# Performance work log

Hardware: AMD Instinct MI355X
Metric: run time of the kernel (lower is better)

The kernel has to match this reference:

```python
import jax, jax.numpy as jnp
import numpy as np

HID = 64
NUM_LAYERS = 2
EPS = 1e-5


def _layernorm(x, g, b):
    mu = jnp.mean(x, axis=-1, keepdims=True)
    var = jnp.mean(jnp.square(x - mu), axis=-1, keepdims=True)
    return (x - mu) * jax.lax.rsqrt(var + EPS) * g + b


def _mlp(x, w1, b1, g, beta, w2, b2):
    # Linear -> LayerNorm -> ReLU -> Linear (torch Linear: x @ W.T + b)
    h = x @ w1.T + b1
    h = jax.nn.relu(_layernorm(h, g, beta))
    return h @ w2.T + b2


def _gru(x, h, wih, whh, bih, bhh):
    # PyTorch GRUCell semantics
    gi = x @ wih.T + bih
    gh = h @ whh.T + bhh
    ir, iz, inn = jnp.split(gi, 3, axis=-1)
    hr, hz, hn = jnp.split(gh, 3, axis=-1)
    r = jax.nn.sigmoid(ir + hr)
    z = jax.nn.sigmoid(iz + hz)
    n = jnp.tanh(inn + r * hn)
    return (1.0 - z) * n + z * h


def setup_inputs() -> dict:
    key = jax.random.key(0)
    ks = iter(jax.random.split(key, 64))
    s = 0.05

    def rn(shape):
        return jax.random.normal(next(ks), shape, dtype=jnp.float32) * s

    B, M, K1 = 32, 256, 128
    inp = {
        'hybrid_input': jax.random.normal(next(ks), (B, M, K1, 4), dtype=jnp.float32),
        'hidden_state': jnp.zeros((B, HID), dtype=jnp.float32),
        # input encoder
        'enc_w1': rn((HID, 4)), 'enc_b1': rn((HID,)),
        'enc_g': jnp.ones((HID,), jnp.float32), 'enc_beta': jnp.zeros((HID,), jnp.float32),
        'enc_w2': rn((HID, HID)), 'enc_b2': rn((HID,)),
        # per-layer, per-side (axis0=layer, axis1=[row,col]) params
        'l_w1': rn((NUM_LAYERS, 2, HID, HID)), 'l_b1': rn((NUM_LAYERS, 2, HID)),
        'l_g': jnp.ones((NUM_LAYERS, 2, HID), jnp.float32), 'l_beta': jnp.zeros((NUM_LAYERS, 2, HID), jnp.float32),
        'l_w2': rn((NUM_LAYERS, 2, HID, HID)), 'l_b2': rn((NUM_LAYERS, 2, HID)),
        'l_gwih': rn((NUM_LAYERS, 2, 3 * HID, HID)), 'l_gwhh': rn((NUM_LAYERS, 2, 3 * HID, HID)),
        'l_gbih': rn((NUM_LAYERS, 2, 3 * HID)), 'l_gbhh': rn((NUM_LAYERS, 2, 3 * HID)),
        # top-level GRU
        'g_wih': rn((3 * HID, HID)), 'g_whh': rn((3 * HID, HID)),
        'g_bih': rn((3 * HID,)), 'g_bhh': rn((3 * HID,)),
        # head: Linear(2H->H) -> ReLU -> Linear(H->1)
        'head_w1': rn((HID, 2 * HID)), 'head_b1': rn((HID,)),
        'head_w2': rn((1, HID)), 'head_b2': rn((1,)),
    }
    return inp


def reference(hybrid_input, hidden_state, enc_w1, enc_b1, enc_g, enc_beta, enc_w2, enc_b2,
              l_w1, l_b1, l_g, l_beta, l_w2, l_b2, l_gwih, l_gwhh, l_gbih, l_gbhh,
              g_wih, g_whh, g_bih, g_bhh, head_w1, head_b1, head_w2, head_b2):
    # input encoder
    x = _mlp(hybrid_input, enc_w1, enc_b1, enc_g, enc_beta, enc_w2, enc_b2)

    for l in range(NUM_LAYERS):
        # row pass: max over axis 2 (K+1)
        row_max = jnp.max(x, axis=2, keepdims=True)
        upd = _mlp(x - row_max, l_w1[l, 0], l_b1[l, 0], l_g[l, 0], l_beta[l, 0], l_w2[l, 0], l_b2[l, 0])
        x = _gru(upd, x, l_gwih[l, 0], l_gwhh[l, 0], l_gbih[l, 0], l_gbhh[l, 0])
        # col pass: max over axis 1 (M)
        col_max = jnp.max(x, axis=1, keepdims=True)
        upd = _mlp(x - col_max, l_w1[l, 1], l_b1[l, 1], l_g[l, 1], l_beta[l, 1], l_w2[l, 1], l_b2[l, 1])
        x = _gru(upd, x, l_gwih[l, 1], l_gwhh[l, 1], l_gbih[l, 1], l_gbhh[l, 1])

    B, M, K1, h = x.shape
    global_feat = jnp.max(x.reshape(B, M * K1, h), axis=1)  # (B, H)
    new_hidden = _gru(global_feat, hidden_state, g_wih, g_whh, g_bih, g_bhh)

    h_exp = jnp.broadcast_to(new_hidden[:, None, None, :], (B, M, K1, h))
    combined = jnp.concatenate([x, h_exp], axis=-1)  # (B, M, K1, 2H)
    hh = jax.nn.relu(combined @ head_w1.T + head_b1)
    logits = (hh @ head_w2.T + head_b2)[..., 0]  # (B, M, K1)
    return logits, new_hidden
```

## Files before the change

kernel.cpp:

```cpp
#include <hip/hip_runtime.h>
#include <math.h>

typedef unsigned int u32;
typedef unsigned short u16;
typedef __attribute__((ext_vector_type(4))) float f32x4;
typedef __attribute__((ext_vector_type(8))) short s16x8;

#define NTOT 1048576
#define SWZ(n, col) ((col) ^ (((n) & 7) << 4))

__device__ __forceinline__ float bflo(u32 v) { return __uint_as_float(v << 16); }
__device__ __forceinline__ float bfhi(u32 v) { return __uint_as_float(v & 0xffff0000u); }
__device__ __forceinline__ u16 f2bf(float f) {
  u32 u = __float_as_uint(f);
  u32 r = ((u >> 16) & 1u) + 0x7fffu;
  return (u16)((u + r) >> 16);
}
__device__ __forceinline__ u32 pk2(float a, float b) {
  return (u32)f2bf(a) | ((u32)f2bf(b) << 16);
}
__device__ __forceinline__ float sigm(float x) {
  return __builtin_amdgcn_rcpf(1.0f + __expf(-x));
}
__device__ __forceinline__ float tanh_f(float x) {
  float e = __expf(2.0f * x);
  return 1.0f - 2.0f * __builtin_amdgcn_rcpf(e + 1.0f);
}
__device__ __forceinline__ float relu(float x) { return fmaxf(x, 0.0f); }

__device__ __forceinline__ void gemm16(const unsigned char* L, int aoff, int boff,
                                       int w, int lq, int lr, f32x4 acc[4]) {
  const int l = lq * 16 + lr;
  const int ws = w & 3, nh = w >> 2;
  s16x8 a0 = *(const s16x8*)(L + aoff + ((ws * 2 + 0) * 64 + l) * 16);
  s16x8 a1 = *(const s16x8*)(L + aoff + ((ws * 2 + 1) * 64 + l) * 16);
  const int c0 = (lq << 4) ^ ((lr & 7) << 4);
  const unsigned char* Bp = L + boff + nh * 8192 + lr * 128;
#pragma unroll
  for (int nt = 0; nt < 4; ++nt) {
    s16x8 b0 = *(const s16x8*)(Bp + nt * 2048 + c0);
    s16x8 b1 = *(const s16x8*)(Bp + nt * 2048 + (c0 ^ 64));
    acc[nt] = __builtin_amdgcn_mfma_f32_16x16x32_bf16(a0, b0, acc[nt], 0, 0, 0);
    acc[nt] = __builtin_amdgcn_mfma_f32_16x16x32_bf16(a1, b1, acc[nt], 0, 0, 0);
  }
}

__device__ __forceinline__ void binit(f32x4 acc[4], float x, float y, float z, float w) {
  f32x4 v; v[0] = x; v[1] = y; v[2] = z; v[3] = w;
#pragma unroll
  for (int nt = 0; nt < 4; ++nt) acc[nt] = v;
}

__global__ void diag_kernel(float* out, float v) { out[0] = v; }

__global__ __launch_bounds__(256) void prep_kernel(
    const float* __restrict__ enc_w2, const float* __restrict__ head_w1,
    const float* __restrict__ l_w1, const float* __restrict__ l_w2,
    const float* __restrict__ l_gwih, const float* __restrict__ l_gwhh,
    ushort* __restrict__ gwF) {
  const int id = blockIdx.x;
  const int t = threadIdx.x;
  const float* src;
  int ld = 64;
  if (id == 0)      { src = enc_w2; }
  else if (id == 1) { src = head_w1; ld = 128; }
  else if (id < 6)  { src = l_w1 + (id - 2) * 4096; }
  else if (id < 10) { src = l_w2 + (id - 6) * 4096; }
  else if (id < 22) { int q = id - 10; src = l_gwih + (q / 3) * 12288 + (q % 3) * 4096; }
  else              { int q = id - 22; src = l_gwhh + (q / 3) * 12288 + (q % 3) * 4096; }
  uint4* dst = (uint4*)(gwF + (size_t)id * 4096);
#pragma unroll
  for (int i = 0; i < 2; ++i) {
    int ch = i * 256 + t;
    int q = ch & 63;
    int g = ch >> 6;
    int j = (g >> 1) * 16 + (q & 15);
    int k = (g & 1) * 32 + (q >> 4) * 8;
    const float* s = src + (size_t)j * ld + k;
    float4 f0 = *(const float4*)(s);
    float4 f1 = *(const float4*)(s + 4);
    uint4 o;
    o.x = pk2(f0.x, f0.y); o.y = pk2(f0.z, f0.w);
    o.z = pk2(f1.x, f1.y); o.w = pk2(f1.z, f1.w);
    dst[ch] = o;
  }
}

__global__ __launch_bounds__(512) void encoder_kernel(
    const float4* __restrict__ hyb, ushort* __restrict__ xG,
    const ushort* __restrict__ gwF, const float* __restrict__ enc_w1,
    const float* __restrict__ b1, const float* __restrict__ gg,
    const float* __restrict__ be, const float* __restrict__ b2,
    float* __restrict__ rmOut) {
  __shared__ __align__(16) unsigned char L[42496];
  const int t = threadIdx.x;
  const int w = t >> 6, l = t & 63, lq = l >> 4, lr = l & 15;
  const int ws = w & 3, nh = w >> 2;
  const int gbase = blockIdx.x * 128;
  const int j0 = ws * 16 + lq * 4;
  const int colb = ws * 32 + lq * 8;

  *(uint4*)(L + 32768 + t * 16) = ((const uint4*)gwF)[t];
  if (t < 256) ((float*)(L + 40960))[t] = enc_w1[t];
  __syncthreads();

  {
    const int n = t >> 2, part = t & 3;
    float4 iv = hyb[gbase + n];
    const float* W1 = (const float*)(L + 40960);
    float h[16];
#pragma unroll
    for (int jj = 0; jj < 16; ++jj) {
      int j = part * 16 + jj;
      float4 wr = *(const float4*)(W1 + j * 4);
      h[jj] = b1[j] + wr.x * iv.x + wr.y * iv.y + wr.z * iv.z + wr.w * iv.w;
    }
    float s = 0.f, q = 0.f;
#pragma unroll
    for (int jj = 0; jj < 16; ++jj) { s += h[jj]; q += h[jj] * h[jj]; }
    s += __shfl_xor(s, 1); q += __shfl_xor(q, 1);
    s += __shfl_xor(s, 2); q += __shfl_xor(q, 2);
    float mean = s * (1.f / 64.f);
    float rstd = rsqrtf(q * (1.f / 64.f) - mean * mean + 1e-5f);
    u32 pk[8];
#pragma unroll
    for (int jj = 0; jj < 16; jj += 2) {
      int j = part * 16 + jj;
      float v0 = relu((h[jj] - mean) * rstd * gg[j] + be[j]);
      float v1 = relu((h[jj + 1] - mean) * rstd * gg[j + 1] + be[j + 1]);
      pk[jj >> 1] = pk2(v0, v1);
    }
    *(uint4*)(L + n * 128 + SWZ(n, part * 32))      = make_uint4(pk[0], pk[1], pk[2], pk[3]);
    *(uint4*)(L + n * 128 + SWZ(n, part * 32 + 16)) = make_uint4(pk[4], pk[5], pk[6], pk[7]);
  }
  __syncthreads();

  float4 vb2 = *(const float4*)(b2 + j0);
  f32x4 acc[4];
  binit(acc, vb2.x, vb2.y, vb2.z, vb2.w);
  gemm16(L, 32768, 0, w, lq, lr, acc);
#pragma unroll
  for (int nt = 0; nt < 4; ++nt) {
    int n = nh * 64 + nt * 16 + lr;
    *(uint2*)(L + 16384 + n * 128 + SWZ(n, colb)) =
        make_uint2(pk2(acc[nt][0], acc[nt][1]), pk2(acc[nt][2], acc[nt][3]));
  }
  {
    float mt[4];
#pragma unroll
    for (int r = 0; r < 4; ++r)
      mt[r] = fmaxf(fmaxf(acc[0][r], acc[1][r]), fmaxf(acc[2][r], acc[3][r]));
#pragma unroll
    for (int m = 1; m < 16; m <<= 1)
#pragma unroll
      for (int r = 0; r < 4; ++r) mt[r] = fmaxf(mt[r], __shfl_xor(mt[r], m));
    if (lr == 0) {
      float4 v; v.x = mt[0]; v.y = mt[1]; v.z = mt[2]; v.w = mt[3];
      *(float4*)(L + 41984 + (nh * 64 + j0) * 4) = v;
    }
  }
  __syncthreads();
  {
    uint4* xout = (uint4*)(xG + (size_t)gbase * 64);
#pragma unroll
    for (int i = 0; i < 2; ++i) {
      int flat = i * 512 + t; int n = flat >> 3, c = flat & 7;
      xout[(size_t)n * 8 + c] = *(const uint4*)(L + 16384 + n * 128 + SWZ(n, c * 16));
    }
  }
  if (t < 64) {
    const float* R = (const float*)(L + 41984);
    rmOut[(size_t)blockIdx.x * 64 + t] = fmaxf(R[t], R[64 + t]);
  }
}

#define PXL 0
#define PP  16384
#define PWB(i) (32768 + (i) * 8192)
#define PRED 65536

__global__ __launch_bounds__(512, 4) void pass_kernel(
    ushort* __restrict__ xG, const ushort* __restrict__ gwF,
    const float* __restrict__ rmG, const float* __restrict__ cmG, int mode,
    int s_w1, int s_w2, int s_ih0, int s_hh0,
    const float* __restrict__ b1, const float* __restrict__ b2,
    const float* __restrict__ gg, const float* __restrict__ be,
    const float* __restrict__ bih, const float* __restrict__ bhh,
    float* __restrict__ rmOut) {
  __shared__ __align__(16) unsigned char L[69632];
  const int t = threadIdx.x;
  const int w = t >> 6, l = t & 63, lq = l >> 4, lr = l & 15;
  const int ws = w & 3, nh = w >> 2;
  const int gbase = blockIdx.x * 128;
  const int j0 = ws * 16 + lq * 4;
  const int colb = ws * 32 + lq * 8;
  const int row = blockIdx.x;
  const int b = gbase >> 15;

  float4 vb1 = *(const float4*)(b1 + j0);
  float4 vg  = *(const float4*)(gg + j0);
  float4 vbe = *(const float4*)(be + j0);
  float4 vb2 = *(const float4*)(b2 + j0);
  float4 bi0 = *(const float4*)(bih + j0),       bh0 = *(const float4*)(bhh + j0);
  float4 bi1 = *(const float4*)(bih + 64 + j0),  bh1 = *(const float4*)(bhh + 64 + j0);
  float4 bi2 = *(const float4*)(bih + 128 + j0), bh2 = *(const float4*)(bhh + 128 + j0);

  {
    int sl[4] = {s_w1, s_w2, s_ih0, s_hh0};
#pragma unroll
    for (int sbi = 0; sbi < 4; ++sbi)
      *(uint4*)(L + PWB(sbi) + t * 16) = ((const uint4*)(gwF + (size_t)sl[sbi] * 4096))[t];
  }
  {
    const uint4* xrow = (const uint4*)(xG + (size_t)gbase * 64);
#pragma unroll
    for (int i = 0; i < 2; ++i) {
      int flat = i * 512 + t; int n = flat >> 3, c = flat & 7;
      uint4 xv = xrow[(size_t)n * 8 + c];
      *(uint4*)(L + PXL + n * 128 + SWZ(n, c * 16)) = xv;
      const float* mvp = (mode == 0) ? (rmG + (size_t)row * 64 + c * 8)
                                     : (cmG + ((size_t)(b * 128 + n)) * 64 + c * 8);
      float4 ma = *(const float4*)(mvp);
      float4 mb = *(const float4*)(mvp + 4);
      uint4 o;
      o.x = pk2(bflo(xv.x) - ma.x, bfhi(xv.x) - ma.y);
      o.y = pk2(bflo(xv.y) - ma.z, bfhi(xv.y) - ma.w);
      o.z = pk2(bflo(xv.z) - mb.x, bfhi(xv.z) - mb.y);
      o.w = pk2(bflo(xv.w) - mb.z, bfhi(xv.w) - mb.w);
      *(uint4*)(L + PP + n * 128 + SWZ(n, c * 16)) = o;
    }
  }
  __syncthreads();

  f32x4 acc[4];
  binit(acc, vb1.x, vb1.y, vb1.z, vb1.w);
  gemm16(L, PWB(0), PP, w, lq, lr, acc);
#pragma unroll
  for (int nt = 0; nt < 4; ++nt) {
    float s = acc[nt][0] + acc[nt][1] + acc[nt][2] + acc[nt][3];
    float q = acc[nt][0] * acc[nt][0] + acc[nt][1] * acc[nt][1] +
              acc[nt][2] * acc[nt][2] + acc[nt][3] * acc[nt][3];
    s += __shfl_xor(s, 16); q += __shfl_xor(q, 16);
    s += __shfl_xor(s, 32); q += __shfl_xor(q, 32);
    if (lq == 0)
      *(float2*)(L + PRED + ((nh * 4 + ws) * 64 + nt * 16 + lr) * 8) = make_float2(s, q);
  }
  __syncthreads();
  {
    *(uint4*)(L + PWB(0) + t * 16) = ((const uint4*)(gwF + (size_t)(s_ih0 + 1) * 4096))[t];
  }
  {
    float gv[4] = {vg.x, vg.y, vg.z, vg.w};
    float bv[4] = {vbe.x, vbe.y, vbe.z, vbe.w};
#pragma unroll
    for (int nt = 0; nt < 4; ++nt) {
      int np = nt * 16 + lr;
      float ss = 0.f, qq = 0.f;
#pragma unroll
      for (int wv = 0; wv < 4; ++wv) {
        float2 pr = *(const float2*)(L + PRED + ((nh * 4 + wv) * 64 + np) * 8);
        ss += pr.x; qq += pr.y;
      }
      float mean = ss * (1.f / 64.f);
      float rstd = rsqrtf(qq * (1.f / 64.f) - mean * mean + 1e-5f);
      float h_[4];
#pragma unroll
      for (int r = 0; r < 4; ++r) h_[r] = relu((acc[nt][r] - mean) * rstd * gv[r] + bv[r]);
      int n = nh * 64 + np;
      *(uint2*)(L + PP + n * 128 + SWZ(n, colb)) =
          make_uint2(pk2(h_[0], h_[1]), pk2(h_[2], h_[3]));
    }
  }
  __syncthreads();

  binit(acc, vb2.x, vb2.y, vb2.z, vb2.w);
  gemm16(L, PWB(1), PP, w, lq, lr, acc);
  __syncthreads();
  {
    *(uint4*)(L + PWB(1) + t * 16) = ((const uint4*)(gwF + (size_t)(s_hh0 + 1) * 4096))[t];
  }
#pragma unroll
  for (int nt = 0; nt < 4; ++nt) {
    int n = nh * 64 + nt * 16 + lr;
    *(uint2*)(L + PP + n * 128 + SWZ(n, colb)) =
        make_uint2(pk2(acc[nt][0], acc[nt][1]), pk2(acc[nt][2], acc[nt][3]));
  }
  __syncthreads();

  binit(acc, bi0.x + bh0.x, bi0.y + bh0.y, bi0.z + bh0.z, bi0.w + bh0.w);
  gemm16(L, PWB(2), PP, w, lq, lr, acc);
  gemm16(L, PWB(3), PXL, w, lq, lr, acc);
  float rg[4][4];
#pragma unroll
  for (int nt = 0; nt < 4; ++nt)
#pragma unroll
    for (int r = 0; r < 4; ++r) rg[nt][r] = sigm(acc[nt][r]);
  __syncthreads();
  {
    *(uint4*)(L + PWB(2) + t * 16) = ((const uint4*)(gwF + (size_t)(s_ih0 + 2) * 4096))[t];
    *(uint4*)(L + PWB(3) + t * 16) = ((const uint4*)(gwF + (size_t)(s_hh0 + 2) * 4096))[t];
  }
  binit(acc, bi1.x + bh1.x, bi1.y + bh1.y, bi1.z + bh1.z, bi1.w + bh1.w);
  gemm16(L, PWB(0), PP, w, lq, lr, acc);
  gemm16(L, PWB(1), PXL, w, lq, lr, acc);
  float zg[4][4];
#pragma unroll
  for (int nt = 0; nt < 4; ++nt)
#pragma unroll
    for (int r = 0; r < 4; ++r) zg[nt][r] = sigm(acc[nt][r]);
  __syncthreads();

  f32x4 ai[4], ah[4];
  binit(ai, bi2.x, bi2.y, bi2.z, bi2.w);
  gemm16(L, PWB(2), PP, w, lq, lr, ai);
  binit(ah, bh2.x, bh2.y, bh2.z, bh2.w);
  gemm16(L, PWB(3), PXL, w, lq, lr, ah);

  float xn[4][4];
#pragma unroll
  for (int nt = 0; nt < 4; ++nt) {
    int n = nh * 64 + nt * 16 + lr;
    uint2 xo = *(const uint2*)(L + PXL + n * 128 + SWZ(n, colb));
    float xv[4] = {bflo(xo.x), bfhi(xo.x), bflo(xo.y), bfhi(xo.y)};
#pragma unroll
    for (int r = 0; r < 4; ++r) {
      float nn = tanh_f(ai[nt][r] + rg[nt][r] * ah[nt][r]);
      xn[nt][r] = nn + zg[nt][r] * (xv[r] - nn);
    }
  }
  __syncthreads();
#pragma unroll
  for (int nt = 0; nt < 4; ++nt) {
    int n = nh * 64 + nt * 16 + lr;
    *(uint2*)(L + PXL + n * 128 + SWZ(n, colb)) =
        make_uint2(pk2(xn[nt][0], xn[nt][1]), pk2(xn[nt][2], xn[nt][3]));
  }
  {
    float mt[4];
#pragma unroll
    for (int r = 0; r < 4; ++r)
      mt[r] = fmaxf(fmaxf(xn[0][r], xn[1][r]), fmaxf(xn[2][r], xn[3][r]));
#pragma unroll
    for (int m = 1; m < 16; m <<= 1)
#pragma unroll
      for (int r = 0; r < 4; ++r) mt[r] = fmaxf(mt[r], __shfl_xor(mt[r], m));
    if (lr == 0) {
      float4 v; v.x = mt[0]; v.y = mt[1]; v.z = mt[2]; v.w = mt[3];
      *(float4*)(L + PRED + (nh * 64 + j0) * 4) = v;
    }
  }
  __syncthreads();
  {
    uint4* xout = (uint4*)(xG + (size_t)gbase * 64);
#pragma unroll
    for (int i = 0; i < 2; ++i) {
      int flat = i * 512 + t; int n = flat >> 3, c = flat & 7;
      xout[(size_t)n * 8 + c] = *(const uint4*)(L + PXL + n * 128 + SWZ(n, c * 16));
    }
  }
  if (t < 64) {
    const float* R = (const float*)(L + PRED);
    rmOut[(size_t)row * 64 + t] = fmaxf(R[t], R[64 + t]);
  }
}

__global__ __launch_bounds__(256) void colmax_kernel(const ushort* __restrict__ xG,
                                                     float* __restrict__ cm) {
  const int t = threadIdx.x;
  const int b = blockIdx.x >> 4, kg = blockIdx.x & 15;
  const int col = t & 31, k1 = kg * 8 + (t >> 5);
  const u32* xu = (const u32*)xG;
  float m0 = -INFINITY, m1 = -INFINITY;
  for (int m = 0; m < 256; ++m) {
    size_t node = ((size_t)(b * 256 + m)) * 128 + k1;
    u32 v = xu[node * 32 + col];
    m0 = fmaxf(m0, bflo(v)); m1 = fmaxf(m1, bfhi(v));
  }
  float* dst = cm + ((size_t)(b * 128 + k1)) * 64 + col * 2;
  dst[0] = m0; dst[1] = m1;
}

__global__ __launch_bounds__(64) void topgru_kernel(
    const float* __restrict__ rm, const float* __restrict__ hs,
    const float* __restrict__ gwih, const float* __restrict__ gwhh,
    const float* __restrict__ gbih, const float* __restrict__ gbhh,
    float* __restrict__ nh, float* __restrict__ outTail) {
  __shared__ float gf[64], h0[64];
  const int b = blockIdx.x, j = threadIdx.x;
  float g0 = -INFINITY, g1 = -INFINITY, g2 = -INFINITY, g3 = -INFINITY;
  const float* base = rm + (size_t)b * 256 * 64 + j;
  for (int r = 0; r < 256; r += 4) {
    g0 = fmaxf(g0, base[(r + 0) * 64]);
    g1 = fmaxf(g1, base[(r + 1) * 64]);
    g2 = fmaxf(g2, base[(r + 2) * 64]);
    g3 = fmaxf(g3, base[(r + 3) * 64]);
  }
  gf[j] = fmaxf(fmaxf(g0, g1), fmaxf(g2, g3));
  h0[j] = hs[b * 64 + j];
  __syncthreads();
  float gi[3], gh[3];
#pragma unroll
  for (int g = 0; g < 3; ++g) {
    float s = gbih[g * 64 + j];
    const float* wr = gwih + (g * 64 + j) * 64;
    for (int k = 0; k < 64; ++k) s += wr[k] * gf[k];
    gi[g] = s;
  }
#pragma unroll
  for (int g = 0; g < 3; ++g) {
    float s = gbhh[g * 64 + j];
    const float* wr = gwhh + (g * 64 + j) * 64;
    for (int k = 0; k < 64; ++k) s += wr[k] * h0[k];
    gh[g] = s;
  }
  float rr = sigm(gi[0] + gh[0]);
  float zz = sigm(gi[1] + gh[1]);
  float nn = tanh_f(gi[2] + rr * gh[2]);
  float val = (1.0f - zz) * nn + zz * h0[j];
  nh[b * 64 + j] = val;
  outTail[b * 64 + j] = val;
}

__global__ __launch_bounds__(64) void hc_kernel(const float* __restrict__ nh,
                                                const float* __restrict__ hw1,
                                                const float* __restrict__ hb1,
                                                float* __restrict__ hc) {
  __shared__ float h0[64];
  const int b = blockIdx.x, j = threadIdx.x;
  h0[j] = nh[b * 64 + j];
  __syncthreads();
  float s = hb1[j];
  const float* wr = hw1 + j * 128 + 64;
  for (int k = 0; k < 64; ++k) s += wr[k] * h0[k];
  hc[b * 64 + j] = s;
}

__global__ __launch_bounds__(256) void head_kernel(
    const ushort* __restrict__ xG, const ushort* __restrict__ gwF,
    const float* __restrict__ hc, const float* __restrict__ hw2,
    const float* __restrict__ hb2, float* __restrict__ out) {
  __shared__ __align__(16) unsigned char L[17408];
  const int t = threadIdx.x;
  const int w = t >> 6, l = t & 63, lq = l >> 4, lr = l & 15;
  const int gbase = blockIdx.x * 64;
  const int b = gbase >> 15;
  const int j0 = w * 16 + lq * 4;

  { const uint4* src = (const uint4*)(gwF + 4096);
    *(uint4*)(L + 8192 + t * 16) = src[t];
    *(uint4*)(L + 8192 + (256 + t) * 16) = src[256 + t]; }
  { const uint4* xrow = (const uint4*)(xG + (size_t)gbase * 64);
#pragma unroll
    for (int i = 0; i < 2; ++i) {
      int flat = i * 256 + t; int n = flat >> 3, c = flat & 7;
      *(uint4*)(L + n * 128 + SWZ(n, c * 16)) = xrow[(size_t)n * 8 + c];
    } }
  __syncthreads();

  float4 vhc = *(const float4*)(hc + b * 64 + j0);
  f32x4 acc[4];
  binit(acc, vhc.x, vhc.y, vhc.z, vhc.w);
  gemm16(L, 8192, 0, w, lq, lr, acc);

  float4 w2v = *(const float4*)(hw2 + j0);
  float w2a[4] = {w2v.x, w2v.y, w2v.z, w2v.w};
#pragma unroll
  for (int nt = 0; nt < 4; ++nt) {
    float p = 0.f;
#pragma unroll
    for (int r = 0; r < 4; ++r) p += w2a[r] * relu(acc[nt][r]);
    p += __shfl_xor(p, 16);
    p += __shfl_xor(p, 32);
    if (lq == 0) ((float*)(L + 16384))[w * 64 + nt * 16 + lr] = p;
  }
  __syncthreads();
  if (t < 64) {
    const float* red = (const float*)(L + 16384);
    out[gbase + t] = red[t] + red[64 + t] + red[128 + t] + red[192 + t] + hb2[0];
  }
}

extern "C" void kernel_launch(void* const* d_in, const int* in_sizes, int n_in,
                              void* d_out, int out_size, void* d_ws, size_t ws_size,
                              hipStream_t stream) {
  const float* hybrid   = (const float*)d_in[0];
  const float* hidden   = (const float*)d_in[1];
  const float* enc_w1   = (const float*)d_in[2];
  const float* enc_b1   = (const float*)d_in[3];
  const float* enc_g    = (const float*)d_in[4];
  const float* enc_beta = (const float*)d_in[5];
  const float* enc_w2   = (const float*)d_in[6];
  const float* enc_b2   = (const float*)d_in[7];
  const float* l_w1     = (const float*)d_in[8];
  const float* l_b1     = (const float*)d_in[9];
  const float* l_g      = (const float*)d_in[10];
  const float* l_beta   = (const float*)d_in[11];
  const float* l_w2     = (const float*)d_in[12];
  const float* l_b2     = (const float*)d_in[13];
  const float* l_gwih   = (const float*)d_in[14];
  const float* l_gwhh   = (const float*)d_in[15];
  const float* l_gbih   = (const float*)d_in[16];
  const float* l_gbhh   = (const float*)d_in[17];
  const float* g_wih    = (const float*)d_in[18];
  const float* g_whh    = (const float*)d_in[19];
  const float* g_bih    = (const float*)d_in[20];
  const float* g_bhh    = (const float*)d_in[21];
  const float* head_w1  = (const float*)d_in[22];
  const float* head_b1  = (const float*)d_in[23];
  const float* head_w2  = (const float*)d_in[24];
  const float* head_b2  = (const float*)d_in[25];

  char* p = (char*)d_ws;
  size_t off = 0;
  auto carve = [&](size_t bytes) { void* r = p + off; off = (off + bytes + 255) & ~255ULL; return r; };
  ushort* xG  = (ushort*)carve((size_t)NTOT * 64 * 2);
  ushort* gwF = (ushort*)carve(34 * 4096 * 2);
  float*  rmG = (float*)carve((size_t)8192 * 64 * 4);
  float*  cmG = (float*)carve((size_t)32 * 128 * 64 * 4);
  float*  nh  = (float*)carve(2048 * 4);
  float*  hcb = (float*)carve(2048 * 4);

  if (ws_size < off) {
    diag_kernel<<<1, 1, 0, stream>>>((float*)d_out, 1.0f + (float)ws_size * 1e-9f);
    return;
  }

  prep_kernel<<<34, 256, 0, stream>>>(enc_w2, head_w1, l_w1, l_w2, l_gwih, l_gwhh, gwF);
  encoder_kernel<<<8192, 512, 0, stream>>>((const float4*)hybrid, xG, gwF, enc_w1,
                                           enc_b1, enc_g, enc_beta, enc_b2, rmG);

  for (int lyr = 0; lyr < 2; ++lyr) {
    for (int s = 0; s < 2; ++s) {
      const int m = lyr * 2 + s;
      if (s == 1) colmax_kernel<<<512, 256, 0, stream>>>(xG, cmG);
      pass_kernel<<<8192, 512, 0, stream>>>(
          xG, gwF, rmG, cmG, s,
          2 + m, 6 + m, 10 + 3 * m, 22 + 3 * m,
          l_b1 + m * 64, l_b2 + m * 64, l_g + m * 64, l_beta + m * 64,
          l_gbih + m * 192, l_gbhh + m * 192, rmG);
    }
  }

  topgru_kernel<<<32, 64, 0, stream>>>(rmG, hidden, g_wih, g_whh, g_bih, g_bhh,
                                       nh, (float*)d_out + 1048576);
  hc_kernel<<<32, 64, 0, stream>>>(nh, head_w1, head_b1, hcb);
  head_kernel<<<16384, 256, 0, stream>>>(xG, gwF, hcb, head_w2, head_b2, (float*)d_out);
}
```

Baseline: 814.2 us.

## Load MFMA weight fragments directly from global memory instead of LDS staging

The weight A-operand fragments are now read straight from global memory (L2-resident, pre-swizzled layout) in each GEMM, so the per-block copies of weights into shared memory and the syncs that guarded reloads are gone. This cuts LDS use in pass_kernel from about 68KB to 36KB, and its launch bound rises to 6 blocks per CU for higher occupancy. The head kernel is reshaped to 512 threads covering 128 rows, matching the pass kernel. The cost is repeated global/L2 loads of weight fragments per wave, which adds latency to each GEMM.

```diff
diff --git a/kernel.cpp b/kernel.cpp
--- a/kernel.cpp
+++ b/kernel.cpp
@@ -28,12 +28,12 @@
 }
 __device__ __forceinline__ float relu(float x) { return fmaxf(x, 0.0f); }
 
-__device__ __forceinline__ void gemm16(const unsigned char* L, int aoff, int boff,
-                                       int w, int lq, int lr, f32x4 acc[4]) {
-  const int l = lq * 16 + lr;
-  const int ws = w & 3, nh = w >> 2;
-  s16x8 a0 = *(const s16x8*)(L + aoff + ((ws * 2 + 0) * 64 + l) * 16);
-  s16x8 a1 = *(const s16x8*)(L + aoff + ((ws * 2 + 1) * 64 + l) * 16);
+__device__ __forceinline__ void gemmG(const ushort* __restrict__ gA,
+                                      const unsigned char* L, int boff,
+                                      int ws, int nh, int l, int lq, int lr,
+                                      f32x4 acc[4]) {
+  s16x8 a0 = *(const s16x8*)(gA + ((ws * 128 + l) << 3));
+  s16x8 a1 = *(const s16x8*)(gA + ((ws * 128 + 64 + l) << 3));
   const int c0 = (lq << 4) ^ ((lr & 7) << 4);
   const unsigned char* Bp = L + boff + nh * 8192 + lr * 128;
 #pragma unroll
@@ -92,7 +92,7 @@
     const float* __restrict__ b1, const float* __restrict__ gg,
     const float* __restrict__ be, const float* __restrict__ b2,
     float* __restrict__ rmOut) {
-  __shared__ __align__(16) unsigned char L[42496];
+  __shared__ __align__(16) unsigned char L[34304];
   const int t = threadIdx.x;
   const int w = t >> 6, l = t & 63, lq = l >> 4, lr = l & 15;
   const int ws = w & 3, nh = w >> 2;
@@ -100,14 +100,13 @@
   const int j0 = ws * 16 + lq * 4;
   const int colb = ws * 32 + lq * 8;
 
-  *(uint4*)(L + 32768 + t * 16) = ((const uint4*)gwF)[t];
-  if (t < 256) ((float*)(L + 40960))[t] = enc_w1[t];
+  if (t < 256) ((float*)(L + 32768))[t] = enc_w1[t];
   __syncthreads();
 
   {
     const int n = t >> 2, part = t & 3;
     float4 iv = hyb[gbase + n];
-    const float* W1 = (const float*)(L + 40960);
+    const float* W1 = (const float*)(L + 32768);
     float h[16];
 #pragma unroll
     for (int jj = 0; jj < 16; ++jj) {
@@ -138,7 +137,7 @@
   float4 vb2 = *(const float4*)(b2 + j0);
   f32x4 acc[4];
   binit(acc, vb2.x, vb2.y, vb2.z, vb2.w);
-  gemm16(L, 32768, 0, w, lq, lr, acc);
+  gemmG(gwF, L, 0, ws, nh, l, lq, lr, acc);
 #pragma unroll
   for (int nt = 0; nt < 4; ++nt) {
     int n = nh * 64 + nt * 16 + lr;
@@ -156,7 +155,7 @@
       for (int r = 0; r < 4; ++r) mt[r] = fmaxf(mt[r], __shfl_xor(mt[r], m));
     if (lr == 0) {
       float4 v; v.x = mt[0]; v.y = mt[1]; v.z = mt[2]; v.w = mt[3];
-      *(float4*)(L + 41984 + (nh * 64 + j0) * 4) = v;
+      *(float4*)(L + 33792 + (nh * 64 + j0) * 4) = v;
     }
   }
   __syncthreads();
@@ -169,17 +168,16 @@
     }
   }
   if (t < 64) {
-    const float* R = (const float*)(L + 41984);
+    const float* R = (const float*)(L + 33792);
     rmOut[(size_t)blockIdx.x * 64 + t] = fmaxf(R[t], R[64 + t]);
   }
 }
 
 #define PXL 0
 #define PP  16384
-#define PWB(i) (32768 + (i) * 8192)
-#define PRED 65536
-
-__global__ __launch_bounds__(512, 4) void pass_kernel(
+#define PRED 32768
+
+__global__ __launch_bounds__(512, 6) void pass_kernel(
     ushort* __restrict__ xG, const ushort* __restrict__ gwF,
     const float* __restrict__ rmG, const float* __restrict__ cmG, int mode,
     int s_w1, int s_w2, int s_ih0, int s_hh0,
@@ -187,7 +185,7 @@
     const float* __restrict__ gg, const float* __restrict__ be,
     const float* __restrict__ bih, const float* __restrict__ bhh,
     float* __restrict__ rmOut) {
-  __shared__ __align__(16) unsigned char L[69632];
+  __shared__ __align__(16) unsigned char L[36864];
   const int t = threadIdx.x;
   const int w = t >> 6, l = t & 63, lq = l >> 4, lr = l & 15;
   const int ws = w & 3, nh = w >> 2;
@@ -197,6 +195,15 @@
   const int row = blockIdx.x;
   const int b = gbase >> 15;
 
+  const ushort* Aw1 = gwF + (size_t)s_w1 * 4096;
+  const ushort* Aw2 = gwF + (size_t)s_w2 * 4096;
+  const ushort* Ai0 = gwF + (size_t)s_ih0 * 4096;
+  const ushort* Ai1 = Ai0 + 4096;
+  const ushort* Ai2 = Ai1 + 4096;
+  const ushort* Ah0 = gwF + (size_t)s_hh0 * 4096;
+  const ushort* Ah1 = Ah0 + 4096;
+  const ushort* Ah2 = Ah1 + 4096;
+
   float4 vb1 = *(const float4*)(b1 + j0);
   float4 vg  = *(const float4*)(gg + j0);
   float4 vbe = *(const float4*)(be + j0);
@@ -205,12 +212,6 @@
   float4 bi1 = *(const float4*)(bih + 64 + j0),  bh1 = *(const float4*)(bhh + 64 + j0);
   float4 bi2 = *(const float4*)(bih + 128 + j0), bh2 = *(const float4*)(bhh + 128 + j0);
 
-  {
-    int sl[4] = {s_w1, s_w2, s_ih0, s_hh0};
-#pragma unroll
-    for (int sbi = 0; sbi < 4; ++sbi)
-      *(uint4*)(L + PWB(sbi) + t * 16) = ((const uint4*)(gwF + (size_t)sl[sbi] * 4096))[t];
-  }
   {
     const uint4* xrow = (const uint4*)(xG + (size_t)gbase * 64);
 #pragma unroll
@@ -234,7 +235,7 @@
 
   f32x4 acc[4];
   binit(acc, vb1.x, vb1.y, vb1.z, vb1.w);
-  gemm16(L, PWB(0), PP, w, lq, lr, acc);
+  gemmG(Aw1, L, PP, ws, nh, l, lq, lr, acc);
 #pragma unroll
   for (int nt = 0; nt < 4; ++nt) {
     float s = acc[nt][0] + acc[nt][1] + acc[nt][2] + acc[nt][3];
@@ -246,9 +247,7 @@
       *(float2*)(L + PRED + ((nh * 4 + ws) * 64 + nt * 16 + lr) * 8) = make_float2(s, q);
   }
   __syncthreads();
-  {
-    *(uint4*)(L + PWB(0) + t * 16) = ((const uint4*)(gwF + (size_t)(s_ih0 + 1) * 4096))[t];
-  }
+
   {
     float gv[4] = {vg.x, vg.y, vg.z, vg.w};
     float bv[4] = {vbe.x, vbe.y, vbe.z, vbe.w};
@@ -274,11 +273,8 @@
   __syncthreads();
 
   binit(acc, vb2.x, vb2.y, vb2.z, vb2.w);
-  gemm16(L, PWB(1), PP, w, lq, lr, acc);
-  __syncthreads();
-  {
-    *(uint4*)(L + PWB(1) + t * 16) = ((const uint4*)(gwF + (size_t)(s_hh0 + 1) * 4096))[t];
-  }
+  gemmG(Aw2, L, PP, ws, nh, l, lq, lr, acc);
+  __syncthreads();
 #pragma unroll
   for (int nt = 0; nt < 4; ++nt) {
     int n = nh * 64 + nt * 16 + lr;
@@ -288,33 +284,28 @@
   __syncthreads();
 
   binit(acc, bi0.x + bh0.x, bi0.y + bh0.y, bi0.z + bh0.z, bi0.w + bh0.w);
-  gemm16(L, PWB(2), PP, w, lq, lr, acc);
-  gemm16(L, PWB(3), PXL, w, lq, lr, acc);
+  gemmG(Ai0, L, PP, ws, nh, l, lq, lr, acc);
+  gemmG(Ah0, L, PXL, ws, nh, l, lq, lr, acc);
   float rg[4][4];
 #pragma unroll
   for (int nt = 0; nt < 4; ++nt)
 #pragma unroll
     for (int r = 0; r < 4; ++r) rg[nt][r] = sigm(acc[nt][r]);
-  __syncthreads();
-  {
-    *(uint4*)(L + PWB(2) + t * 16) = ((const uint4*)(gwF + (size_t)(s_ih0 + 2) * 4096))[t];
-    *(uint4*)(L + PWB(3) + t * 16) = ((const uint4*)(gwF + (size_t)(s_hh0 + 2) * 4096))[t];
-  }
+
   binit(acc, bi1.x + bh1.x, bi1.y + bh1.y, bi1.z + bh1.z, bi1.w + bh1.w);
-  gemm16(L, PWB(0), PP, w, lq, lr, acc);
-  gemm16(L, PWB(1), PXL, w, lq, lr, acc);
+  gemmG(Ai1, L, PP, ws, nh, l, lq, lr, acc);
+  gemmG(Ah1, L, PXL, ws, nh, l, lq, lr, acc);
   float zg[4][4];
 #pragma unroll
   for (int nt = 0; nt < 4; ++nt)
 #pragma unroll
     for (int r = 0; r < 4; ++r) zg[nt][r] = sigm(acc[nt][r]);
-  __syncthreads();
 
   f32x4 ai[4], ah[4];
   binit(ai, bi2.x, bi2.y, bi2.z, bi2.w);
-  gemm16(L, PWB(2), PP, w, lq, lr, ai);
+  gemmG(Ai2, L, PP, ws, nh, l, lq, lr, ai);
   binit(ah, bh2.x, bh2.y, bh2.z, bh2.w);
-  gemm16(L, PWB(3), PXL, w, lq, lr, ah);
+  gemmG(Ah2, L, PXL, ws, nh, l, lq, lr, ah);
 
   float xn[4][4];
 #pragma unroll
@@ -435,24 +426,22 @@
   hc[b * 64 + j] = s;
 }
 
-__global__ __launch_bounds__(256) void head_kernel(
+__global__ __launch_bounds__(512) void head_kernel(
     const ushort* __restrict__ xG, const ushort* __restrict__ gwF,
     const float* __restrict__ hc, const float* __restrict__ hw2,
     const float* __restrict__ hb2, float* __restrict__ out) {
-  __shared__ __align__(16) unsigned char L[17408];
+  __shared__ __align__(16) unsigned char L[18432];
   const int t = threadIdx.x;
   const int w = t >> 6, l = t & 63, lq = l >> 4, lr = l & 15;
-  const int gbase = blockIdx.x * 64;
+  const int ws = w & 3, nh = w >> 2;
+  const int gbase = blockIdx.x * 128;
   const int b = gbase >> 15;
-  const int j0 = w * 16 + lq * 4;
-
-  { const uint4* src = (const uint4*)(gwF + 4096);
-    *(uint4*)(L + 8192 + t * 16) = src[t];
-    *(uint4*)(L + 8192 + (256 + t) * 16) = src[256 + t]; }
+  const int j0 = ws * 16 + lq * 4;
+
   { const uint4* xrow = (const uint4*)(xG + (size_t)gbase * 64);
 #pragma unroll
     for (int i = 0; i < 2; ++i) {
-      int flat = i * 256 + t; int n = flat >> 3, c = flat & 7;
+      int flat = i * 512 + t; int n = flat >> 3, c = flat & 7;
       *(uint4*)(L + n * 128 + SWZ(n, c * 16)) = xrow[(size_t)n * 8 + c];
     } }
   __syncthreads();
@@ -460,7 +449,7 @@
   float4 vhc = *(const float4*)(hc + b * 64 + j0);
   f32x4 acc[4];
   binit(acc, vhc.x, vhc.y, vhc.z, vhc.w);
-  gemm16(L, 8192, 0, w, lq, lr, acc);
+  gemmG(gwF + 4096, L, 0, ws, nh, l, lq, lr, acc);
 
   float4 w2v = *(const float4*)(hw2 + j0);
   float w2a[4] = {w2v.x, w2v.y, w2v.z, w2v.w};
@@ -471,12 +460,12 @@
     for (int r = 0; r < 4; ++r) p += w2a[r] * relu(acc[nt][r]);
     p += __shfl_xor(p, 16);
     p += __shfl_xor(p, 32);
-    if (lq == 0) ((float*)(L + 16384))[w * 64 + nt * 16 + lr] = p;
-  }
-  __syncthreads();
-  if (t < 64) {
-    const float* red = (const float*)(L + 16384);
-    out[gbase + t] = red[t] + red[64 + t] + red[128 + t] + red[192 + t] + hb2[0];
+    if (lq == 0) ((float*)(L + 16384))[(nh * 4 + ws) * 64 + nt * 16 + lr] = p;
+  }
+  __syncthreads();
+  if (t < 128) {
+    const float* red = (const float*)(L + 16384) + (t >> 6) * 256 + (t & 63);
+    out[gbase + t] = red[0] + red[64] + red[128] + red[192] + hb2[0];
   }
 }
 
@@ -544,5 +533,5 @@
   topgru_kernel<<<32, 64, 0, stream>>>(rmG, hidden, g_wih, g_whh, g_bih, g_bhh,
                                        nh, (float*)d_out + 1048576);
   hc_kernel<<<32, 64, 0, stream>>>(nh, head_w1, head_b1, hcb);
-  head_kernel<<<16384, 256, 0, stream>>>(xG, gwF, hcb, head_w2, head_b2, (float*)d_out);
-}
+  head_kernel<<<8192, 512, 0, stream>>>(xG, gwF, hcb, head_w2, head_b2, (float*)d_out);
+}
```

Result: slower. 1.190 ms (+46.1%).
